# Performance work log

Hardware: AMD Instinct MI355X
Metric: run time of the kernel (lower is better)

Reference implementation:

```python
import jax, jax.numpy as jnp
import numpy as np

B, C_IN, C_MID, C_OUT, H, W = 16, 128, 128, 128, 128, 128
DN = ('NCHW', 'OIHW', 'NCHW')


def conv1x1(x, w, b):
    y = jax.lax.conv_general_dilated(x, w, (1, 1), 'VALID', dimension_numbers=DN)
    return y + b[None, :, None, None]


def dwconv3(x, w, b):
    # depthwise 3x3, padding=1, groups = channels
    y = jax.lax.conv_general_dilated(x, w, (1, 1), ((1, 1), (1, 1)),
                                     feature_group_count=x.shape[1],
                                     dimension_numbers=DN)
    return y + b[None, :, None, None]


def setup_inputs() -> dict:
    key = jax.random.key(0)
    ks = jax.random.split(key, 15)
    s = 0.05
    return {
        'x':   jax.random.normal(ks[0], (B, C_IN, H, W), jnp.float32),
        'qw':  jax.random.normal(ks[1], (C_MID, C_IN, 1, 1), jnp.float32) * s,
        'qb':  jax.random.normal(ks[2], (C_MID,), jnp.float32) * s,
        'qdw': jax.random.normal(ks[3], (C_MID, 1, 3, 3), jnp.float32) * s,
        'qdb': jax.random.normal(ks[4], (C_MID,), jnp.float32) * s,
        'kw':  jax.random.normal(ks[5], (C_MID, C_IN, 1, 1), jnp.float32) * s,
        'kb':  jax.random.normal(ks[6], (C_MID,), jnp.float32) * s,
        'kdw': jax.random.normal(ks[7], (C_MID, 1, 3, 3), jnp.float32) * s,
        'kdb': jax.random.normal(ks[8], (C_MID,), jnp.float32) * s,
        'vw':  jax.random.normal(ks[9], (C_MID, C_IN, 1, 1), jnp.float32) * s,
        'vb':  jax.random.normal(ks[10], (C_MID,), jnp.float32) * s,
        'vdw': jax.random.normal(ks[11], (C_MID, 1, 3, 3), jnp.float32) * s,
        'vdb': jax.random.normal(ks[12], (C_MID,), jnp.float32) * s,
        'aw':  jax.random.normal(ks[13], (C_OUT, C_MID, 1, 1), jnp.float32) * s,
        'ab':  jax.random.normal(ks[14], (C_OUT,), jnp.float32) * s,
    }


def reference(x, qw, qb, qdw, qdb, kw, kb, kdw, kdb, vw, vb, vdw, vdb, aw, ab):
    b, c, h, w = x.shape
    q = dwconv3(conv1x1(x, qw, qb), qdw, qdb)
    k = dwconv3(conv1x1(x, kw, kb), kdw, kdb)
    v = dwconv3(conv1x1(x, vw, vb), vdw, vdb)
    # b c h w -> b c (h w)
    q = q.reshape(b, -1, h * w)
    k = k.reshape(b, -1, h * w)
    v = v.reshape(b, -1, h * w)
    # L2-normalize over spatial dim (torch F.normalize: x / max(||x||, eps))
    eps = 1e-12
    q = q / jnp.maximum(jnp.linalg.norm(q, axis=-1, keepdims=True), eps)
    k = k / jnp.maximum(jnp.linalg.norm(k, axis=-1, keepdims=True), eps)
    # channel-wise attention: [b, c, c]
    a = jax.nn.softmax(jnp.einsum('bcn,bdn->bcd', q, k), axis=-1)
    out = jnp.einsum('bcd,bdn->bcn', a, v).reshape(b, -1, h, w)
    return conv1x1(out, aw, ab)
```

## Files before the change

kernel.cpp:

```cpp
#include <hip/hip_runtime.h>

typedef unsigned short u16;
typedef unsigned int u32;
typedef __attribute__((ext_vector_type(8))) __bf16 bf16x8;
typedef __attribute__((ext_vector_type(4))) float f32x4;
typedef __attribute__((ext_vector_type(4))) u32 u32x4;
typedef __attribute__((ext_vector_type(2))) u32 u32x2;

#define HW 16384
#define C 128
#define NB 16
#define LSTR 136

__device__ __forceinline__ u16 f2bf(float f) {
    __bf16 h = (__bf16)f;
    union { __bf16 h; u16 u; } c; c.h = h; return c.u;
}
__device__ __forceinline__ float bf2f(u16 u) {
    union { u32 i; float f; } c; c.i = ((u32)u) << 16; return c.f;
}
__device__ __forceinline__ float bflo(u32 w) { return bf2f((u16)(w & 0xffffu)); }
__device__ __forceinline__ float bfhi(u32 w) { return bf2f((u16)(w >> 16)); }

__device__ __forceinline__ void load_af(
    const u16* __restrict__ W, bf16x8 (&af)[2][4], int wave, int m_lo, int quad)
{
    #pragma unroll
    for (int mt = 0; mt < 2; ++mt)
        #pragma unroll
        for (int ks = 0; ks < 4; ++ks) {
            int m = wave * 32 + mt * 16 + m_lo;
            af[mt][ks] = *(const bf16x8*)(W + (size_t)m * 128 + ks * 32 + quad * 8);
        }
}

__device__ __forceinline__ void mfma_tile2(
    const bf16x8 (&af)[2][4], const u16* lds,
    f32x4 (&acc)[2][8], int m_lo, int quad)
{
    #pragma unroll
    for (int mt = 0; mt < 2; ++mt)
        #pragma unroll
        for (int nt = 0; nt < 8; ++nt) {
            f32x4 z = {0.f, 0.f, 0.f, 0.f};
            acc[mt][nt] = z;
        }
    #pragma unroll
    for (int ks = 0; ks < 4; ++ks) {
        #pragma unroll
        for (int nt = 0; nt < 8; ++nt) {
            int n  = nt * 16 + m_lo;
            int cs = (ks * 4 + quad) ^ ((n >> 2) & 7);
            bf16x8 bfrag = *(const bf16x8*)(lds + n * LSTR + cs * 8);
            acc[0][nt] = __builtin_amdgcn_mfma_f32_16x16x32_bf16(bfrag, af[0][ks], acc[0][nt], 0, 0, 0);
            acc[1][nt] = __builtin_amdgcn_mfma_f32_16x16x32_bf16(bfrag, af[1][ks], acc[1][nt], 0, 0, 0);
        }
    }
}

__global__ __launch_bounds__(256) void k_wcvt(
    const float* __restrict__ qw, const float* __restrict__ kw,
    const float* __restrict__ vw, u16* __restrict__ wbf)
{
    int m = blockIdx.x;
    const float* src = m == 0 ? qw : (m == 1 ? kw : vw);
    u16* dst = wbf + (size_t)m * 16384;
    #pragma unroll
    for (int i = 0; i < 16; ++i) {
        int idx = threadIdx.x + 256 * i;
        f32x4 v = *(const f32x4*)(src + idx * 4);
        u32x2 p;
        p.x = (u32)f2bf(v[0]) | ((u32)f2bf(v[1]) << 16);
        p.y = (u32)f2bf(v[2]) | ((u32)f2bf(v[3]) << 16);
        *(u32x2*)(dst + idx * 4) = p;
    }
}

__global__ __launch_bounds__(256) void k_conv_qkv(
    float* __restrict__ x, const u16* __restrict__ wbf,
    const float* __restrict__ qbi, const float* __restrict__ kbi,
    const float* __restrict__ vbi,
    u16* __restrict__ qpl, u16* __restrict__ kpl)
{
    __shared__ __align__(16) u16 lds[128 * LSTR];
    const int tid  = threadIdx.x;
    const int lane = tid & 63;
    const int wave = tid >> 6;
    const int m_lo = lane & 15;
    const int quad = lane >> 4;
    const int b  = blockIdx.z;
    const int n0 = blockIdx.x * 128;
    float* Xb = x + (size_t)b * C * HW;

    {
        f32x4 v[2][8];
        #pragma unroll
        for (int r = 0; r < 2; ++r) {
            int idx = tid + 256 * r;
            int n4  = idx & 31;
            int kc  = idx >> 5;
            const float* src = Xb + (size_t)(kc * 8) * HW + n0 + n4 * 4;
            #pragma unroll
            for (int j = 0; j < 8; ++j) v[r][j] = *(const f32x4*)(src + (size_t)j * HW);
        }
        #pragma unroll
        for (int r = 0; r < 2; ++r) {
            int idx = tid + 256 * r;
            int n4  = idx & 31;
            int kc  = idx >> 5;
            #pragma unroll
            for (int t = 0; t < 4; ++t) {
                union { u16 u[8]; u32x4 q; } e;
                #pragma unroll
                for (int j = 0; j < 8; ++j) e.u[j] = f2bf(v[r][j][t]);
                int row = n4 * 4 + t;
                int cs  = kc ^ (n4 & 7);
                *(u32x4*)(lds + row * LSTR + cs * 8) = e.q;
            }
        }
    }
    __syncthreads();

    const u16* wq = wbf;
    const u16* wk = wbf + 16384;
    const u16* wv = wbf + 32768;
    u16* Yq = qpl + (size_t)b * C * HW;
    u16* Yk = kpl + (size_t)b * C * HW;

    bf16x8 af[2][4];
    f32x4 acc[2][8];

    load_af(wq, af, wave, m_lo, quad);
    mfma_tile2(af, lds, acc, m_lo, quad);
    #pragma unroll
    for (int mt = 0; mt < 2; ++mt) {
        int m = wave * 32 + mt * 16 + m_lo;
        float bm = qbi[m];
        u16* rowp = Yq + (size_t)m * HW + n0 + quad * 4;
        #pragma unroll
        for (int nt = 0; nt < 8; ++nt) {
            u32x2 pr;
            pr.x = (u32)f2bf(acc[mt][nt][0] + bm) | ((u32)f2bf(acc[mt][nt][1] + bm) << 16);
            pr.y = (u32)f2bf(acc[mt][nt][2] + bm) | ((u32)f2bf(acc[mt][nt][3] + bm) << 16);
            *(u32x2*)(rowp + nt * 16) = pr;
        }
    }

    load_af(wk, af, wave, m_lo, quad);
    mfma_tile2(af, lds, acc, m_lo, quad);
    #pragma unroll
    for (int mt = 0; mt < 2; ++mt) {
        int m = wave * 32 + mt * 16 + m_lo;
        float bm = kbi[m];
        u16* rowp = Yk + (size_t)m * HW + n0 + quad * 4;
        #pragma unroll
        for (int nt = 0; nt < 8; ++nt) {
            u32x2 pr;
            pr.x = (u32)f2bf(acc[mt][nt][0] + bm) | ((u32)f2bf(acc[mt][nt][1] + bm) << 16);
            pr.y = (u32)f2bf(acc[mt][nt][2] + bm) | ((u32)f2bf(acc[mt][nt][3] + bm) << 16);
            *(u32x2*)(rowp + nt * 16) = pr;
        }
    }

    load_af(wv, af, wave, m_lo, quad);
    mfma_tile2(af, lds, acc, m_lo, quad);
    #pragma unroll
    for (int mt = 0; mt < 2; ++mt) {
        int m = wave * 32 + mt * 16 + m_lo;
        float bm = vbi[m];
        float* rowp = Xb + (size_t)m * HW + n0 + quad * 4;
        #pragma unroll
        for (int nt = 0; nt < 8; ++nt) {
            f32x4 o = acc[mt][nt];
            o[0] += bm; o[1] += bm; o[2] += bm; o[3] += bm;
            *(f32x4*)(rowp + nt * 16) = o;
        }
    }
}

__global__ __launch_bounds__(256) void k_dw_qk(
    u16* __restrict__ qpl, u16* __restrict__ kpl,
    const float* __restrict__ qdw, const float* __restrict__ qdb,
    const float* __restrict__ kdw, const float* __restrict__ kdb,
    float* __restrict__ norm2)
{
    __shared__ __align__(16) u16 pl[HW + 8];
    __shared__ float red[256];
    int pid = blockIdx.x;
    int s = pid >> 11, bc = pid & 2047, c = bc & 127;
    u16* plane = (s ? kpl : qpl) + (size_t)bc * HW;
    const float* dw = (s ? kdw : qdw) + c * 9;
    float bias = (s ? kdb : qdb)[c];
    int tid = threadIdx.x;

    #pragma unroll
    for (int i = 0; i < 8; ++i) {
        int idx = tid + 256 * i;
        *(u32x4*)(pl + idx * 8) = *(const u32x4*)(plane + idx * 8);
    }
    if (tid < 4) *(u32*)(pl + HW + tid * 2) = 0u;
    float w[9];
    #pragma unroll
    for (int j = 0; j < 9; ++j) w[j] = dw[j];
    __syncthreads();

    float ssq = 0.f;
    #pragma unroll 1
    for (int i = 0; i < 8; ++i) {
        int p0 = (tid + 256 * i) * 8;
        int py = p0 >> 7, px0 = p0 & 127;
        bool lok = px0 > 0, rok = px0 < 120;
        float nb[3][10];
        #pragma unroll
        for (int dy = 0; dy < 3; ++dy) {
            int yy = py + dy - 1;
            bool yok = (yy >= 0) && (yy < 128);
            int ya = yok ? yy : 0;
            const u16* rp = pl + ya * 128;
            u32x2 L  = *(const u32x2*)(rp + (lok ? px0 - 4 : 0));
            u32x2 M0 = *(const u32x2*)(rp + px0);
            u32x2 M1 = *(const u32x2*)(rp + px0 + 4);
            u32x2 R  = *(const u32x2*)(rp + px0 + 8);
            float rm = yok ? 1.f : 0.f;
            nb[dy][0] = (lok && yok) ? bfhi(L.y) : 0.f;
            nb[dy][1] = bflo(M0.x) * rm;
            nb[dy][2] = bfhi(M0.x) * rm;
            nb[dy][3] = bflo(M0.y) * rm;
            nb[dy][4] = bfhi(M0.y) * rm;
            nb[dy][5] = bflo(M1.x) * rm;
            nb[dy][6] = bfhi(M1.x) * rm;
            nb[dy][7] = bflo(M1.y) * rm;
            nb[dy][8] = bfhi(M1.y) * rm;
            nb[dy][9] = (rok && yok) ? bflo(R.x) : 0.f;
        }
        u16 o[8];
        #pragma unroll
        for (int t = 0; t < 8; ++t) {
            float acc = bias;
            #pragma unroll
            for (int dy = 0; dy < 3; ++dy)
                #pragma unroll
                for (int dx = 0; dx < 3; ++dx)
                    acc += w[dy * 3 + dx] * nb[dy][t + dx];
            ssq += acc * acc;
            o[t] = f2bf(acc);
        }
        u32x4 pr;
        pr.x = (u32)o[0] | ((u32)o[1] << 16);
        pr.y = (u32)o[2] | ((u32)o[3] << 16);
        pr.z = (u32)o[4] | ((u32)o[5] << 16);
        pr.w = (u32)o[6] | ((u32)o[7] << 16);
        *(u32x4*)(plane + p0) = pr;
    }
    red[tid] = ssq;
    __syncthreads();
    for (int off = 128; off > 0; off >>= 1) {
        if (tid < off) red[tid] += red[tid + off];
        __syncthreads();
    }
    if (tid == 0) norm2[s * (NB * C) + bc] = red[0];
}

__global__ __launch_bounds__(256) void k_gram(
    const u16* __restrict__ q, const u16* __restrict__ k, float* __restrict__ G)
{
    int kz = blockIdx.x, nz = blockIdx.y, b = blockIdx.z;
    const u16* qb = q + (size_t)b * C * HW;
    const u16* kb = k + (size_t)b * C * HW;
    int lane = threadIdx.x & 63, wave = threadIdx.x >> 6;
    int m_lo = lane & 15, quad = lane >> 4;
    f32x4 acc[2][4];
    #pragma unroll
    for (int mt = 0; mt < 2; ++mt)
        #pragma unroll
        for (int nt = 0; nt < 4; ++nt) {
            f32x4 z = {0.f, 0.f, 0.f, 0.f};
            acc[mt][nt] = z;
        }
    #pragma unroll 4
    for (int step = 0; step < 16; ++step) {
        int kk = kz * 512 + step * 32 + quad * 8;
        bf16x8 a0 = *(const bf16x8*)(qb + (size_t)(wave * 32 + m_lo) * HW + kk);
        bf16x8 a1 = *(const bf16x8*)(qb + (size_t)(wave * 32 + 16 + m_lo) * HW + kk);
        #pragma unroll
        for (int nt = 0; nt < 4; ++nt) {
            bf16x8 bf = *(const bf16x8*)(kb + (size_t)(nz * 64 + nt * 16 + m_lo) * HW + kk);
            acc[0][nt] = __builtin_amdgcn_mfma_f32_16x16x32_bf16(a0, bf, acc[0][nt], 0, 0, 0);
            acc[1][nt] = __builtin_amdgcn_mfma_f32_16x16x32_bf16(a1, bf, acc[1][nt], 0, 0, 0);
        }
    }
    float* Gb = G + (size_t)b * C * C;
    #pragma unroll
    for (int mt = 0; mt < 2; ++mt)
        #pragma unroll
        for (int nt = 0; nt < 4; ++nt)
            #pragma unroll
            for (int r = 0; r < 4; ++r) {
                int m = wave * 32 + mt * 16 + quad * 4 + r;
                int n = nz * 64 + nt * 16 + m_lo;
                atomicAdd(&Gb[m * C + n], acc[mt][nt][r]);
            }
}

__global__ __launch_bounds__(128) void k_softmax(float* __restrict__ G, const float* __restrict__ norm2)
{
    __shared__ float red[128];
    int c = blockIdx.x, b = blockIdx.y, d = threadIdx.x;
    float* row = G + ((size_t)b * C + c) * C;
    float nq = fmaxf(sqrtf(norm2[b * C + c]), 1e-12f);
    float nk = fmaxf(sqrtf(norm2[NB * C + b * C + d]), 1e-12f);
    float sv = row[d] / (nq * nk);
    red[d] = sv; __syncthreads();
    for (int off = 64; off > 0; off >>= 1) {
        if (d < off) red[d] = fmaxf(red[d], red[d + off]);
        __syncthreads();
    }
    float mx = red[0]; __syncthreads();
    float e = __expf(sv - mx);
    red[d] = e; __syncthreads();
    for (int off = 64; off > 0; off >>= 1) {
        if (d < off) red[d] += red[d + off];
        __syncthreads();
    }
    row[d] = e / red[0];
}

__global__ __launch_bounds__(256) void k_mproj(
    const float* __restrict__ G, const float* __restrict__ aw, u16* __restrict__ M)
{
    __shared__ float As[128 * 16];
    int b = blockIdx.y, d0 = blockIdx.x * 16, tid = threadIdx.x;
    const float* A = G + (size_t)b * C * C;
    #pragma unroll
    for (int i = 0; i < 8; ++i) {
        int idx = tid + 256 * i;
        int cc = idx >> 4, dd = idx & 15;
        As[idx] = A[cc * C + d0 + dd];
    }
    __syncthreads();
    #pragma unroll
    for (int i = 0; i < 8; ++i) {
        int idx = tid + 256 * i;
        int oo = idx >> 4, dd = idx & 15;
        float s = 0.f;
        for (int cc = 0; cc < 128; ++cc)
            s += aw[oo * C + cc] * As[cc * 16 + dd];
        M[((size_t)b * C + oo) * C + d0 + dd] = f2bf(s);
    }
}

__global__ __launch_bounds__(256) void k_out(
    const u16* __restrict__ M, const float* __restrict__ v,
    const float* __restrict__ vdw, const float* __restrict__ vdb,
    const float* __restrict__ ab, float* __restrict__ out)
{
    __shared__ __align__(16) u16 lds[128 * LSTR];
    const int tid  = threadIdx.x;
    const int lane = tid & 63;
    const int wave = tid >> 6;
    const int m_lo = lane & 15;
    const int quad = lane >> 4;
    const int b   = blockIdx.z;
    const int row = blockIdx.x;
    const int n0  = row * 128;
    const float* Vb = v + (size_t)b * C * HW;

    int rs[3] = { row > 0 ? row - 1 : 0, row, row < 127 ? row + 1 : 127 };
    float rmask[3] = { row > 0 ? 1.f : 0.f, 1.f, row < 127 ? 1.f : 0.f };

    #pragma unroll
    for (int it = 0; it < 2; ++it) {
        int idx = tid + 256 * it;
        int n8 = idx & 15;
        int kq = idx >> 4;
        int p0 = n8 * 8;
        float lm  = (n8 > 0)  ? 1.f : 0.f;
        float rmx = (n8 < 15) ? 1.f : 0.f;
        int pL = (n8 > 0)  ? p0 - 1 : 0;
        int pR = (n8 < 15) ? p0 + 8 : 127;
        float o[4][8];
        #pragma unroll
        for (int j = 0; j < 4; ++j) {
            int ch = kq * 4 + j;
            const float* pw = vdw + ch * 9;
            float bias = vdb[ch];
            const float* plane = Vb + (size_t)ch * HW;
            f32x4 m0[3], m1[3];
            float eL[3], eR[3];
            #pragma unroll
            for (int dy = 0; dy < 3; ++dy) {
                const float* rp = plane + rs[dy] * 128;
                m0[dy] = *(const f32x4*)(rp + p0);
                m1[dy] = *(const f32x4*)(rp + p0 + 4);
                eL[dy] = rp[pL];
                eR[dy] = rp[pR];
            }
            #pragma unroll
            for (int t = 0; t < 8; ++t) o[j][t] = bias;
            #pragma unroll
            for (int dy = 0; dy < 3; ++dy) {
                float rm = rmask[dy];
                float win[10];
                win[0] = eL[dy] * lm * rm;
                win[9] = eR[dy] * rmx * rm;
                #pragma unroll
                for (int q2 = 0; q2 < 4; ++q2) { win[1 + q2] = m0[dy][q2] * rm; win[5 + q2] = m1[dy][q2] * rm; }
                float w0 = pw[dy * 3 + 0], w1 = pw[dy * 3 + 1], w2 = pw[dy * 3 + 2];
                #pragma unroll
                for (int t = 0; t < 8; ++t)
                    o[j][t] += w0 * win[t] + w1 * win[t + 1] + w2 * win[t + 2];
            }
        }
        #pragma unroll
        for (int t = 0; t < 8; ++t) {
            int rw  = p0 + t;
            int n4t = (rw >> 2) & 31;
            int cs  = (kq >> 1) ^ (n4t & 7);
            u32x2 e;
            e.x = (u32)f2bf(o[0][t]) | ((u32)f2bf(o[1][t]) << 16);
            e.y = (u32)f2bf(o[2][t]) | ((u32)f2bf(o[3][t]) << 16);
            *(u32x2*)(lds + rw * LSTR + cs * 8 + (kq & 1) * 4) = e;
        }
    }
    __syncthreads();

    bf16x8 af[2][4];
    f32x4 acc[2][8];
    load_af(M + (size_t)b * C * C, af, wave, m_lo, quad);
    mfma_tile2(af, lds, acc, m_lo, quad);

    float* Ob = out + (size_t)b * C * HW;
    #pragma unroll
    for (int mt = 0; mt < 2; ++mt) {
        int m = wave * 32 + mt * 16 + m_lo;
        float bm = ab[m];
        float* rowp = Ob + (size_t)m * HW + n0 + quad * 4;
        #pragma unroll
        for (int nt = 0; nt < 8; ++nt) {
            f32x4 o = acc[mt][nt];
            o[0] += bm; o[1] += bm; o[2] += bm; o[3] += bm;
            *(f32x4*)(rowp + nt * 16) = o;
        }
    }
}

extern "C" void kernel_launch(void* const* d_in, const int* in_sizes, int n_in,
                              void* d_out, int out_size, void* d_ws, size_t ws_size,
                              hipStream_t stream)
{
    float* x         = (float*)d_in[0];
    const float* qw  = (const float*)d_in[1];
    const float* qbi = (const float*)d_in[2];
    const float* qdw = (const float*)d_in[3];
    const float* qdb = (const float*)d_in[4];
    const float* kw  = (const float*)d_in[5];
    const float* kbi = (const float*)d_in[6];
    const float* kdw = (const float*)d_in[7];
    const float* kdb = (const float*)d_in[8];
    const float* vw  = (const float*)d_in[9];
    const float* vbi = (const float*)d_in[10];
    const float* vdw = (const float*)d_in[11];
    const float* vdb = (const float*)d_in[12];
    const float* aw  = (const float*)d_in[13];
    const float* ab  = (const float*)d_in[14];

    u16* qpl = (u16*)d_out;
    u16* kpl = qpl + (size_t)NB * C * HW;

    float* G     = (float*)d_ws;
    float* norm2 = G + (size_t)NB * C * C;
    u16*   M     = (u16*)(norm2 + 2 * NB * C);
    u16*   wbf   = M + (size_t)NB * C * C;

    hipMemsetAsync(G, 0, (size_t)NB * C * C * sizeof(float), stream);

    k_wcvt<<<dim3(3), 256, 0, stream>>>(qw, kw, vw, wbf);
    k_conv_qkv<<<dim3(HW / 128, 1, NB), 256, 0, stream>>>(x, wbf, qbi, kbi, vbi, qpl, kpl);
    k_dw_qk<<<dim3(2 * NB * C), 256, 0, stream>>>(qpl, kpl, qdw, qdb, kdw, kdb, norm2);
    k_gram<<<dim3(32, 2, NB), 256, 0, stream>>>(qpl, kpl, G);
    k_softmax<<<dim3(C, NB), 128, 0, stream>>>(G, norm2);
    k_mproj<<<dim3(8, NB), 256, 0, stream>>>(G, aw, M);
    k_out<<<dim3(HW / 128, 1, NB), 256, 0, stream>>>(M, x, vdw, vdb, ab, (float*)d_out);
}
```

Measured before the change: 554.3 us.

## Stage x tile via async global-to-LDS loads and shuffle depthwise halos

The QKV conv kernel now loads the fp32 input tile straight into shared memory with global_load_lds (16-byte async copies), then reads it from LDS for the bf16 conversion and swizzled store. The LDS buffer is enlarged to 64KB to hold the fp32 tile. Separately, the depthwise conv in the V path takes its left and right halo pixels from neighbouring lanes via warp shuffles instead of extra scalar global loads. The trade-off is higher LDS use, which may cut occupancy, plus added barriers.

```diff
diff --git a/kernel.cpp b/kernel.cpp
--- a/kernel.cpp
+++ b/kernel.cpp
@@ -21,6 +21,12 @@
 }
 __device__ __forceinline__ float bflo(u32 w) { return bf2f((u16)(w & 0xffffu)); }
 __device__ __forceinline__ float bfhi(u32 w) { return bf2f((u16)(w >> 16)); }
+
+__device__ __forceinline__ void async_load16(const void* g, void* l) {
+    __builtin_amdgcn_global_load_lds(
+        (const __attribute__((address_space(1))) unsigned int*)g,
+        (__attribute__((address_space(3))) unsigned int*)l, 16, 0, 0);
+}
 
 __device__ __forceinline__ void load_af(
     const u16* __restrict__ W, bf16x8 (&af)[2][4], int wave, int m_lo, int quad)
@@ -82,7 +88,9 @@
     const float* __restrict__ vbi,
     u16* __restrict__ qpl, u16* __restrict__ kpl)
 {
-    __shared__ __align__(16) u16 lds[128 * LSTR];
+    __shared__ __align__(16) u32 smem[16384];
+    u16*   lds  = (u16*)smem;
+    float* ldsf = (float*)smem;
     const int tid  = threadIdx.x;
     const int lane = tid & 63;
     const int wave = tid >> 6;
@@ -93,16 +101,29 @@
     float* Xb = x + (size_t)b * C * HW;
 
     {
+        const float* gb = Xb + n0;
+        #pragma unroll
+        for (int j = 0; j < 16; ++j) {
+            int Rj = wave * 16 + j;
+            int krow = 2 * Rj + (lane >> 5);
+            const float* src = gb + (size_t)krow * HW + (lane & 31) * 4;
+            async_load16(src, (char*)smem + (size_t)Rj * 1024);
+        }
+    }
+    __syncthreads();
+
+    {
         f32x4 v[2][8];
         #pragma unroll
         for (int r = 0; r < 2; ++r) {
             int idx = tid + 256 * r;
             int n4  = idx & 31;
             int kc  = idx >> 5;
-            const float* src = Xb + (size_t)(kc * 8) * HW + n0 + n4 * 4;
-            #pragma unroll
-            for (int j = 0; j < 8; ++j) v[r][j] = *(const f32x4*)(src + (size_t)j * HW);
-        }
+            #pragma unroll
+            for (int j = 0; j < 8; ++j)
+                v[r][j] = *(const f32x4*)(ldsf + (size_t)(kc * 8 + j) * 128 + n4 * 4);
+        }
+        __syncthreads();
         #pragma unroll
         for (int r = 0; r < 2; ++r) {
             int idx = tid + 256 * r;
@@ -376,33 +397,30 @@
         int p0 = n8 * 8;
         float lm  = (n8 > 0)  ? 1.f : 0.f;
         float rmx = (n8 < 15) ? 1.f : 0.f;
-        int pL = (n8 > 0)  ? p0 - 1 : 0;
-        int pR = (n8 < 15) ? p0 + 8 : 127;
         float o[4][8];
         #pragma unroll
         for (int j = 0; j < 4; ++j) {
             int ch = kq * 4 + j;
-            const float* pw = vdw + ch * 9;
-            float bias = vdb[ch];
             const float* plane = Vb + (size_t)ch * HW;
             f32x4 m0[3], m1[3];
-            float eL[3], eR[3];
             #pragma unroll
             for (int dy = 0; dy < 3; ++dy) {
                 const float* rp = plane + rs[dy] * 128;
                 m0[dy] = *(const f32x4*)(rp + p0);
                 m1[dy] = *(const f32x4*)(rp + p0 + 4);
-                eL[dy] = rp[pL];
-                eR[dy] = rp[pR];
             }
+            const float* pw = vdw + ch * 9;
+            float bias = vdb[ch];
             #pragma unroll
             for (int t = 0; t < 8; ++t) o[j][t] = bias;
             #pragma unroll
             for (int dy = 0; dy < 3; ++dy) {
                 float rm = rmask[dy];
+                float lval = __shfl_up(m1[dy][3], 1);
+                float rval = __shfl_down(m0[dy][0], 1);
                 float win[10];
-                win[0] = eL[dy] * lm * rm;
-                win[9] = eR[dy] * rmx * rm;
+                win[0] = lval * lm * rm;
+                win[9] = rval * rmx * rm;
                 #pragma unroll
                 for (int q2 = 0; q2 < 4; ++q2) { win[1 + q2] = m0[dy][q2] * rm; win[5 + q2] = m1[dy][q2] * rm; }
                 float w0 = pw[dy * 3 + 0], w1 = pw[dy * 3 + 1], w2 = pw[dy * 3 + 2];
```

Measured after the change: 526.6 us. -5.0%, faster.

## Fuse 1x1 conv with depthwise conv via row-halo recompute for q/k and v

Applied to the files above, without the earlier changes.

Replaces the separate 1x1-conv and depthwise-conv kernels with fused kernels. Each block stages three input rows, recomputes the 1x1 conv for each row with MFMA and folds the 3x3 depthwise taps in registers, using lane shuffles for the horizontal neighbours. Q and K norms are accumulated with atomics. The V path is recomputed inside the output kernel, so the fp32 V plane is no longer written to and re-read from global memory. The cost is three times the 1x1-conv MFMA work, larger LDS use (three tiles per block, which lowers occupancy), and cross-block atomics for the norms.

```diff
diff --git a/kernel.cpp b/kernel.cpp
--- a/kernel.cpp
+++ b/kernel.cpp
@@ -16,11 +16,6 @@
     __bf16 h = (__bf16)f;
     union { __bf16 h; u16 u; } c; c.h = h; return c.u;
 }
-__device__ __forceinline__ float bf2f(u16 u) {
-    union { u32 i; float f; } c; c.i = ((u32)u) << 16; return c.f;
-}
-__device__ __forceinline__ float bflo(u32 w) { return bf2f((u16)(w & 0xffffu)); }
-__device__ __forceinline__ float bfhi(u32 w) { return bf2f((u16)(w >> 16)); }
 
 __device__ __forceinline__ void load_af(
     const u16* __restrict__ W, bf16x8 (&af)[2][4], int wave, int m_lo, int quad)
@@ -54,6 +49,66 @@
             bf16x8 bfrag = *(const bf16x8*)(lds + n * LSTR + cs * 8);
             acc[0][nt] = __builtin_amdgcn_mfma_f32_16x16x32_bf16(bfrag, af[0][ks], acc[0][nt], 0, 0, 0);
             acc[1][nt] = __builtin_amdgcn_mfma_f32_16x16x32_bf16(bfrag, af[1][ks], acc[1][nt], 0, 0, 0);
+        }
+    }
+}
+
+__device__ __forceinline__ void stage_row(
+    const float* __restrict__ Xb, int rowIdx, u16* xt, int tid)
+{
+    f32x4 v[2][8];
+    #pragma unroll
+    for (int r = 0; r < 2; ++r) {
+        int idx = tid + 256 * r;
+        int n4  = idx & 31;
+        int kc  = idx >> 5;
+        const float* src = Xb + (size_t)(kc * 8) * HW + rowIdx * 128 + n4 * 4;
+        #pragma unroll
+        for (int j = 0; j < 8; ++j) v[r][j] = *(const f32x4*)(src + (size_t)j * HW);
+    }
+    #pragma unroll
+    for (int r = 0; r < 2; ++r) {
+        int idx = tid + 256 * r;
+        int n4  = idx & 31;
+        int kc  = idx >> 5;
+        #pragma unroll
+        for (int t = 0; t < 4; ++t) {
+            union { u16 u[8]; u32x4 q; } e;
+            #pragma unroll
+            for (int j = 0; j < 8; ++j) e.u[j] = f2bf(v[r][j][t]);
+            int row = n4 * 4 + t;
+            int cs  = kc ^ (n4 & 7);
+            *(u32x4*)(xt + row * LSTR + cs * 8) = e.q;
+        }
+    }
+}
+
+__device__ __forceinline__ void fold_dw(
+    const f32x4 (&acc)[2][8], float (&oacc)[2][8][4],
+    const float (&cbias)[2], const float (&dww)[2][9],
+    int dr, float rm, int lane, int quad)
+{
+    #pragma unroll
+    for (int mt = 0; mt < 2; ++mt) {
+        float cbm = cbias[mt];
+        float w0 = dww[mt][dr * 3 + 0], w1 = dww[mt][dr * 3 + 1], w2 = dww[mt][dr * 3 + 2];
+        #pragma unroll
+        for (int nt = 0; nt < 8; ++nt) {
+            float c0 = acc[mt][nt][0] + cbm;
+            float c1 = acc[mt][nt][1] + cbm;
+            float c2 = acc[mt][nt][2] + cbm;
+            float c3 = acc[mt][nt][3] + cbm;
+            float xl = (quad == 3) ? (acc[mt][(nt + 7) & 7][3] + cbm) : c3;
+            float xr = (quad == 0) ? (acc[mt][(nt + 1) & 7][0] + cbm) : c0;
+            float lv = __shfl(xl, (lane + 48) & 63);
+            float rv = __shfl(xr, (lane + 16) & 63);
+            if (nt == 0) lv = (quad == 0) ? 0.f : lv;
+            if (nt == 7) rv = (quad == 3) ? 0.f : rv;
+            float g0 = lv * rm, g1 = c0 * rm, g2 = c1 * rm, g3 = c2 * rm, g4 = c3 * rm, g5 = rv * rm;
+            oacc[mt][nt][0] += w0 * g0 + w1 * g1 + w2 * g2;
+            oacc[mt][nt][1] += w0 * g1 + w1 * g2 + w2 * g3;
+            oacc[mt][nt][2] += w0 * g2 + w1 * g3 + w2 * g4;
+            oacc[mt][nt][3] += w0 * g3 + w1 * g4 + w2 * g5;
         }
     }
 }
@@ -76,189 +131,89 @@
     }
 }
 
-__global__ __launch_bounds__(256) void k_conv_qkv(
-    float* __restrict__ x, const u16* __restrict__ wbf,
+__global__ __launch_bounds__(256) void k_qk_fused(
+    const float* __restrict__ x, const u16* __restrict__ wbf,
     const float* __restrict__ qbi, const float* __restrict__ kbi,
-    const float* __restrict__ vbi,
-    u16* __restrict__ qpl, u16* __restrict__ kpl)
-{
-    __shared__ __align__(16) u16 lds[128 * LSTR];
+    const float* __restrict__ qdw, const float* __restrict__ qdb,
+    const float* __restrict__ kdw, const float* __restrict__ kdb,
+    u16* __restrict__ qpl, u16* __restrict__ kpl, float* __restrict__ norm2)
+{
+    __shared__ __align__(16) u16 xs[3][128 * LSTR];
     const int tid  = threadIdx.x;
     const int lane = tid & 63;
     const int wave = tid >> 6;
     const int m_lo = lane & 15;
     const int quad = lane >> 4;
-    const int b  = blockIdx.z;
-    const int n0 = blockIdx.x * 128;
-    float* Xb = x + (size_t)b * C * HW;
-
-    {
-        f32x4 v[2][8];
-        #pragma unroll
-        for (int r = 0; r < 2; ++r) {
-            int idx = tid + 256 * r;
-            int n4  = idx & 31;
-            int kc  = idx >> 5;
-            const float* src = Xb + (size_t)(kc * 8) * HW + n0 + n4 * 4;
-            #pragma unroll
-            for (int j = 0; j < 8; ++j) v[r][j] = *(const f32x4*)(src + (size_t)j * HW);
-        }
-        #pragma unroll
-        for (int r = 0; r < 2; ++r) {
-            int idx = tid + 256 * r;
-            int n4  = idx & 31;
-            int kc  = idx >> 5;
-            #pragma unroll
-            for (int t = 0; t < 4; ++t) {
-                union { u16 u[8]; u32x4 q; } e;
+    const int b = blockIdx.z;
+    const int r = blockIdx.x;
+    const int n0 = r * 128;
+    const float* Xb = x + (size_t)b * C * HW;
+
+    int rs[3] = { r > 0 ? r - 1 : 0, r, r < 127 ? r + 1 : 127 };
+    float rmask[3] = { r > 0 ? 1.f : 0.f, 1.f, r < 127 ? 1.f : 0.f };
+
+    stage_row(Xb, rs[0], xs[0], tid);
+    stage_row(Xb, rs[1], xs[1], tid);
+    stage_row(Xb, rs[2], xs[2], tid);
+    __syncthreads();
+
+    #pragma unroll 1
+    for (int sp = 0; sp < 2; ++sp) {
+        const u16* W      = wbf + sp * 16384;
+        const float* cbp  = sp ? kbi : qbi;
+        const float* dwWp = sp ? kdw : qdw;
+        const float* dwBp = sp ? kdb : qdb;
+        u16* Y = (sp ? kpl : qpl) + (size_t)b * C * HW;
+
+        bf16x8 af[2][4];
+        load_af(W, af, wave, m_lo, quad);
+        float cbias[2], dww[2][9];
+        #pragma unroll
+        for (int mt = 0; mt < 2; ++mt) {
+            int m = wave * 32 + mt * 16 + m_lo;
+            cbias[mt] = cbp[m];
+            #pragma unroll
+            for (int j = 0; j < 9; ++j) dww[mt][j] = dwWp[m * 9 + j];
+        }
+
+        float oacc[2][8][4];
+        #pragma unroll
+        for (int mt = 0; mt < 2; ++mt)
+            #pragma unroll
+            for (int nt = 0; nt < 8; ++nt)
                 #pragma unroll
-                for (int j = 0; j < 8; ++j) e.u[j] = f2bf(v[r][j][t]);
-                int row = n4 * 4 + t;
-                int cs  = kc ^ (n4 & 7);
-                *(u32x4*)(lds + row * LSTR + cs * 8) = e.q;
+                for (int rr = 0; rr < 4; ++rr) oacc[mt][nt][rr] = 0.f;
+
+        f32x4 acc[2][8];
+        #pragma unroll
+        for (int dr = 0; dr < 3; ++dr) {
+            mfma_tile2(af, xs[dr], acc, m_lo, quad);
+            fold_dw(acc, oacc, cbias, dww, dr, rmask[dr], lane, quad);
+        }
+
+        #pragma unroll
+        for (int mt = 0; mt < 2; ++mt) {
+            int m = wave * 32 + mt * 16 + m_lo;
+            float b2 = dwBp[m];
+            u16* rowp = Y + (size_t)m * HW + n0 + quad * 4;
+            float sq = 0.f;
+            #pragma unroll
+            for (int nt = 0; nt < 8; ++nt) {
+                float o0 = oacc[mt][nt][0] + b2;
+                float o1 = oacc[mt][nt][1] + b2;
+                float o2 = oacc[mt][nt][2] + b2;
+                float o3 = oacc[mt][nt][3] + b2;
+                sq += o0 * o0 + o1 * o1 + o2 * o2 + o3 * o3;
+                u32x2 pr;
+                pr.x = (u32)f2bf(o0) | ((u32)f2bf(o1) << 16);
+                pr.y = (u32)f2bf(o2) | ((u32)f2bf(o3) << 16);
+                *(u32x2*)(rowp + nt * 16) = pr;
             }
-        }
-    }
-    __syncthreads();
-
-    const u16* wq = wbf;
-    const u16* wk = wbf + 16384;
-    const u16* wv = wbf + 32768;
-    u16* Yq = qpl + (size_t)b * C * HW;
-    u16* Yk = kpl + (size_t)b * C * HW;
-
-    bf16x8 af[2][4];
-    f32x4 acc[2][8];
-
-    load_af(wq, af, wave, m_lo, quad);
-    mfma_tile2(af, lds, acc, m_lo, quad);
-    #pragma unroll
-    for (int mt = 0; mt < 2; ++mt) {
-        int m = wave * 32 + mt * 16 + m_lo;
-        float bm = qbi[m];
-        u16* rowp = Yq + (size_t)m * HW + n0 + quad * 4;
-        #pragma unroll
-        for (int nt = 0; nt < 8; ++nt) {
-            u32x2 pr;
-            pr.x = (u32)f2bf(acc[mt][nt][0] + bm) | ((u32)f2bf(acc[mt][nt][1] + bm) << 16);
-            pr.y = (u32)f2bf(acc[mt][nt][2] + bm) | ((u32)f2bf(acc[mt][nt][3] + bm) << 16);
-            *(u32x2*)(rowp + nt * 16) = pr;
-        }
-    }
-
-    load_af(wk, af, wave, m_lo, quad);
-    mfma_tile2(af, lds, acc, m_lo, quad);
-    #pragma unroll
-    for (int mt = 0; mt < 2; ++mt) {
-        int m = wave * 32 + mt * 16 + m_lo;
-        float bm = kbi[m];
-        u16* rowp = Yk + (size_t)m * HW + n0 + quad * 4;
-        #pragma unroll
-        for (int nt = 0; nt < 8; ++nt) {
-            u32x2 pr;
-            pr.x = (u32)f2bf(acc[mt][nt][0] + bm) | ((u32)f2bf(acc[mt][nt][1] + bm) << 16);
-            pr.y = (u32)f2bf(acc[mt][nt][2] + bm) | ((u32)f2bf(acc[mt][nt][3] + bm) << 16);
-            *(u32x2*)(rowp + nt * 16) = pr;
-        }
-    }
-
-    load_af(wv, af, wave, m_lo, quad);
-    mfma_tile2(af, lds, acc, m_lo, quad);
-    #pragma unroll
-    for (int mt = 0; mt < 2; ++mt) {
-        int m = wave * 32 + mt * 16 + m_lo;
-        float bm = vbi[m];
-        float* rowp = Xb + (size_t)m * HW + n0 + quad * 4;
-        #pragma unroll
-        for (int nt = 0; nt < 8; ++nt) {
-            f32x4 o = acc[mt][nt];
-            o[0] += bm; o[1] += bm; o[2] += bm; o[3] += bm;
-            *(f32x4*)(rowp + nt * 16) = o;
-        }
-    }
-}
-
-__global__ __launch_bounds__(256) void k_dw_qk(
-    u16* __restrict__ qpl, u16* __restrict__ kpl,
-    const float* __restrict__ qdw, const float* __restrict__ qdb,
-    const float* __restrict__ kdw, const float* __restrict__ kdb,
-    float* __restrict__ norm2)
-{
-    __shared__ __align__(16) u16 pl[HW + 8];
-    __shared__ float red[256];
-    int pid = blockIdx.x;
-    int s = pid >> 11, bc = pid & 2047, c = bc & 127;
-    u16* plane = (s ? kpl : qpl) + (size_t)bc * HW;
-    const float* dw = (s ? kdw : qdw) + c * 9;
-    float bias = (s ? kdb : qdb)[c];
-    int tid = threadIdx.x;
-
-    #pragma unroll
-    for (int i = 0; i < 8; ++i) {
-        int idx = tid + 256 * i;
-        *(u32x4*)(pl + idx * 8) = *(const u32x4*)(plane + idx * 8);
-    }
-    if (tid < 4) *(u32*)(pl + HW + tid * 2) = 0u;
-    float w[9];
-    #pragma unroll
-    for (int j = 0; j < 9; ++j) w[j] = dw[j];
-    __syncthreads();
-
-    float ssq = 0.f;
-    #pragma unroll 1
-    for (int i = 0; i < 8; ++i) {
-        int p0 = (tid + 256 * i) * 8;
-        int py = p0 >> 7, px0 = p0 & 127;
-        bool lok = px0 > 0, rok = px0 < 120;
-        float nb[3][10];
-        #pragma unroll
-        for (int dy = 0; dy < 3; ++dy) {
-            int yy = py + dy - 1;
-            bool yok = (yy >= 0) && (yy < 128);
-            int ya = yok ? yy : 0;
-            const u16* rp = pl + ya * 128;
-            u32x2 L  = *(const u32x2*)(rp + (lok ? px0 - 4 : 0));
-            u32x2 M0 = *(const u32x2*)(rp + px0);
-            u32x2 M1 = *(const u32x2*)(rp + px0 + 4);
-            u32x2 R  = *(const u32x2*)(rp + px0 + 8);
-            float rm = yok ? 1.f : 0.f;
-            nb[dy][0] = (lok && yok) ? bfhi(L.y) : 0.f;
-            nb[dy][1] = bflo(M0.x) * rm;
-            nb[dy][2] = bfhi(M0.x) * rm;
-            nb[dy][3] = bflo(M0.y) * rm;
-            nb[dy][4] = bfhi(M0.y) * rm;
-            nb[dy][5] = bflo(M1.x) * rm;
-            nb[dy][6] = bfhi(M1.x) * rm;
-            nb[dy][7] = bflo(M1.y) * rm;
-            nb[dy][8] = bfhi(M1.y) * rm;
-            nb[dy][9] = (rok && yok) ? bflo(R.x) : 0.f;
-        }
-        u16 o[8];
-        #pragma unroll
-        for (int t = 0; t < 8; ++t) {
-            float acc = bias;
-            #pragma unroll
-            for (int dy = 0; dy < 3; ++dy)
-                #pragma unroll
-                for (int dx = 0; dx < 3; ++dx)
-                    acc += w[dy * 3 + dx] * nb[dy][t + dx];
-            ssq += acc * acc;
-            o[t] = f2bf(acc);
-        }
-        u32x4 pr;
-        pr.x = (u32)o[0] | ((u32)o[1] << 16);
-        pr.y = (u32)o[2] | ((u32)o[3] << 16);
-        pr.z = (u32)o[4] | ((u32)o[5] << 16);
-        pr.w = (u32)o[6] | ((u32)o[7] << 16);
-        *(u32x4*)(plane + p0) = pr;
-    }
-    red[tid] = ssq;
-    __syncthreads();
-    for (int off = 128; off > 0; off >>= 1) {
-        if (tid < off) red[tid] += red[tid + off];
-        __syncthreads();
-    }
-    if (tid == 0) norm2[s * (NB * C) + bc] = red[0];
+            sq += __shfl_xor(sq, 16);
+            sq += __shfl_xor(sq, 32);
+            if (quad == 0) atomicAdd(&norm2[sp * (NB * C) + b * C + m], sq);
+        }
+    }
 }
 
 __global__ __launch_bounds__(256) void k_gram(
@@ -295,10 +250,10 @@
         #pragma unroll
         for (int nt = 0; nt < 4; ++nt)
             #pragma unroll
-            for (int r = 0; r < 4; ++r) {
-                int m = wave * 32 + mt * 16 + quad * 4 + r;
+            for (int rr = 0; rr < 4; ++rr) {
+                int m = wave * 32 + mt * 16 + quad * 4 + rr;
                 int n = nz * 64 + nt * 16 + m_lo;
-                atomicAdd(&Gb[m * C + n], acc[mt][nt][r]);
+                atomicAdd(&Gb[m * C + n], acc[mt][nt][rr]);
             }
 }
 
@@ -349,85 +304,79 @@
     }
 }
 
-__global__ __launch_bounds__(256) void k_out(
-    const u16* __restrict__ M, const float* __restrict__ v,
-    const float* __restrict__ vdw, const float* __restrict__ vdb,
+__global__ __launch_bounds__(256) void k_out_fused(
+    const u16* __restrict__ M, const float* __restrict__ x, const u16* __restrict__ wbf,
+    const float* __restrict__ vbi, const float* __restrict__ vdw, const float* __restrict__ vdb,
     const float* __restrict__ ab, float* __restrict__ out)
 {
-    __shared__ __align__(16) u16 lds[128 * LSTR];
+    __shared__ __align__(16) u16 xs[3][128 * LSTR];
     const int tid  = threadIdx.x;
     const int lane = tid & 63;
     const int wave = tid >> 6;
     const int m_lo = lane & 15;
     const int quad = lane >> 4;
-    const int b   = blockIdx.z;
-    const int row = blockIdx.x;
-    const int n0  = row * 128;
-    const float* Vb = v + (size_t)b * C * HW;
-
-    int rs[3] = { row > 0 ? row - 1 : 0, row, row < 127 ? row + 1 : 127 };
-    float rmask[3] = { row > 0 ? 1.f : 0.f, 1.f, row < 127 ? 1.f : 0.f };
-
-    #pragma unroll
-    for (int it = 0; it < 2; ++it) {
-        int idx = tid + 256 * it;
-        int n8 = idx & 15;
-        int kq = idx >> 4;
-        int p0 = n8 * 8;
-        float lm  = (n8 > 0)  ? 1.f : 0.f;
-        float rmx = (n8 < 15) ? 1.f : 0.f;
-        int pL = (n8 > 0)  ? p0 - 1 : 0;
-        int pR = (n8 < 15) ? p0 + 8 : 127;
-        float o[4][8];
-        #pragma unroll
-        for (int j = 0; j < 4; ++j) {
-            int ch = kq * 4 + j;
-            const float* pw = vdw + ch * 9;
-            float bias = vdb[ch];
-            const float* plane = Vb + (size_t)ch * HW;
-            f32x4 m0[3], m1[3];
-            float eL[3], eR[3];
-            #pragma unroll
-            for (int dy = 0; dy < 3; ++dy) {
-                const float* rp = plane + rs[dy] * 128;
-                m0[dy] = *(const f32x4*)(rp + p0);
-                m1[dy] = *(const f32x4*)(rp + p0 + 4);
-                eL[dy] = rp[pL];
-                eR[dy] = rp[pR];
+    const int b = blockIdx.z;
+    const int r = blockIdx.x;
+    const int n0 = r * 128;
+    const float* Xb = x + (size_t)b * C * HW;
+
+    int rs[3] = { r > 0 ? r - 1 : 0, r, r < 127 ? r + 1 : 127 };
+    float rmask[3] = { r > 0 ? 1.f : 0.f, 1.f, r < 127 ? 1.f : 0.f };
+
+    stage_row(Xb, rs[0], xs[0], tid);
+    stage_row(Xb, rs[1], xs[1], tid);
+    stage_row(Xb, rs[2], xs[2], tid);
+    __syncthreads();
+
+    const u16* wv = wbf + 32768;
+    bf16x8 af[2][4];
+    load_af(wv, af, wave, m_lo, quad);
+    float cbias[2], dww[2][9];
+    #pragma unroll
+    for (int mt = 0; mt < 2; ++mt) {
+        int m = wave * 32 + mt * 16 + m_lo;
+        cbias[mt] = vbi[m];
+        #pragma unroll
+        for (int j = 0; j < 9; ++j) dww[mt][j] = vdw[m * 9 + j];
+    }
+
+    float oacc[2][8][4];
+    #pragma unroll
+    for (int mt = 0; mt < 2; ++mt)
+        #pragma unroll
+        for (int nt = 0; nt < 8; ++nt)
+            #pragma unroll
+            for (int rr = 0; rr < 4; ++rr) oacc[mt][nt][rr] = 0.f;
+
+    f32x4 acc[2][8];
+    #pragma unroll
+    for (int dr = 0; dr < 3; ++dr) {
+        mfma_tile2(af, xs[dr], acc, m_lo, quad);
+        fold_dw(acc, oacc, cbias, dww, dr, rmask[dr], lane, quad);
+    }
+    __syncthreads();
+
+    u16* bt = xs[0];
+    #pragma unroll
+    for (int mt = 0; mt < 2; ++mt) {
+        int m = wave * 32 + mt * 16 + m_lo;
+        int khi = m >> 3, klo = m & 7;
+        float b2 = vdb[m];
+        #pragma unroll
+        for (int nt = 0; nt < 8; ++nt) {
+            int cs = khi ^ ((nt * 4 + quad) & 7);
+            #pragma unroll
+            for (int rr = 0; rr < 4; ++rr) {
+                int px = nt * 16 + quad * 4 + rr;
+                bt[px * LSTR + cs * 8 + klo] = f2bf(oacc[mt][nt][rr] + b2);
             }
-            #pragma unroll
-            for (int t = 0; t < 8; ++t) o[j][t] = bias;
-            #pragma unroll
-            for (int dy = 0; dy < 3; ++dy) {
-                float rm = rmask[dy];
-                float win[10];
-                win[0] = eL[dy] * lm * rm;
-                win[9] = eR[dy] * rmx * rm;
-                #pragma unroll
-                for (int q2 = 0; q2 < 4; ++q2) { win[1 + q2] = m0[dy][q2] * rm; win[5 + q2] = m1[dy][q2] * rm; }
-                float w0 = pw[dy * 3 + 0], w1 = pw[dy * 3 + 1], w2 = pw[dy * 3 + 2];
-                #pragma unroll
-                for (int t = 0; t < 8; ++t)
-                    o[j][t] += w0 * win[t] + w1 * win[t + 1] + w2 * win[t + 2];
-            }
-        }
-        #pragma unroll
-        for (int t = 0; t < 8; ++t) {
-            int rw  = p0 + t;
-            int n4t = (rw >> 2) & 31;
-            int cs  = (kq >> 1) ^ (n4t & 7);
-            u32x2 e;
-            e.x = (u32)f2bf(o[0][t]) | ((u32)f2bf(o[1][t]) << 16);
-            e.y = (u32)f2bf(o[2][t]) | ((u32)f2bf(o[3][t]) << 16);
-            *(u32x2*)(lds + rw * LSTR + cs * 8 + (kq & 1) * 4) = e;
         }
     }
     __syncthreads();
 
-    bf16x8 af[2][4];
-    f32x4 acc[2][8];
-    load_af(M + (size_t)b * C * C, af, wave, m_lo, quad);
-    mfma_tile2(af, lds, acc, m_lo, quad);
+    bf16x8 afm[2][4];
+    load_af(M + (size_t)b * C * C, afm, wave, m_lo, quad);
+    mfma_tile2(afm, bt, acc, m_lo, quad);
 
     float* Ob = out + (size_t)b * C * HW;
     #pragma unroll
@@ -448,7 +397,7 @@
                               void* d_out, int out_size, void* d_ws, size_t ws_size,
                               hipStream_t stream)
 {
-    float* x         = (float*)d_in[0];
+    const float* x   = (const float*)d_in[0];
     const float* qw  = (const float*)d_in[1];
     const float* qbi = (const float*)d_in[2];
     const float* qdw = (const float*)d_in[3];
@@ -472,13 +421,13 @@
     u16*   M     = (u16*)(norm2 + 2 * NB * C);
     u16*   wbf   = M + (size_t)NB * C * C;
 
-    hipMemsetAsync(G, 0, (size_t)NB * C * C * sizeof(float), stream);
+    hipMemsetAsync(G, 0, ((size_t)NB * C * C + 2 * NB * C) * sizeof(float), stream);
 
     k_wcvt<<<dim3(3), 256, 0, stream>>>(qw, kw, vw, wbf);
-    k_conv_qkv<<<dim3(HW / 128, 1, NB), 256, 0, stream>>>(x, wbf, qbi, kbi, vbi, qpl, kpl);
-    k_dw_qk<<<dim3(2 * NB * C), 256, 0, stream>>>(qpl, kpl, qdw, qdb, kdw, kdb, norm2);
+    k_qk_fused<<<dim3(128, 1, NB), 256, 0, stream>>>(
+        x, wbf, qbi, kbi, qdw, qdb, kdw, kdb, qpl, kpl, norm2);
     k_gram<<<dim3(32, 2, NB), 256, 0, stream>>>(qpl, kpl, G);
     k_softmax<<<dim3(C, NB), 128, 0, stream>>>(G, norm2);
     k_mproj<<<dim3(8, NB), 256, 0, stream>>>(G, aw, M);
-    k_out<<<dim3(HW / 128, 1, NB), 256, 0, stream>>>(M, x, vdw, vdb, ab, (float*)d_out);
-}
+    k_out_fused<<<dim3(128, 1, NB), 256, 0, stream>>>(M, x, wbf, vbi, vdw, vdb, ab, (float*)d_out);
+}
```

After: 935.3 us. +68.7%, slower.
